# Kernel tuning notes

Hardware: AMD Instinct MI355X
Metric: run time of the kernel (lower is better)

## Reference

```python
import jax, jax.numpy as jnp
import numpy as np

LN_EPS = 1e-5


def _make_valid_boxes(key, shape):
    # boxes in [x_min, y_min, x_max, y_max] with min < max
    k1, k2 = jax.random.split(key)
    mins = jax.random.uniform(k1, shape, dtype=jnp.float32)            # [.., 2]
    sizes = jax.random.uniform(k2, shape, dtype=jnp.float32) * 0.2 + 1e-3
    return jnp.concatenate([mins, mins + sizes], axis=-1)


def setup_inputs() -> dict:
    key = jax.random.key(0)
    k_t, k_b, k_w = jax.random.split(key, 3)
    N, H = 100000, 768
    target = _make_valid_boxes(k_t, (2,))          # [4]
    ocr_boxes = _make_valid_boxes(k_b, (N, 2))     # [N, 4]
    W = jax.random.normal(k_w, (11, H), dtype=jnp.float32) * (1.0 / np.sqrt(11))
    b = jnp.zeros((H,), dtype=jnp.float32)
    ln_gamma = jnp.ones((H,), dtype=jnp.float32)
    ln_beta = jnp.zeros((H,), dtype=jnp.float32)
    return {"target": target, "ocr_boxes": ocr_boxes, "W": W, "b": b,
            "ln_gamma": ln_gamma, "ln_beta": ln_beta}


def _geo_features(target, boxes):
    # target: [4], boxes: [N, 4]  (x_min, y_min, x_max, y_max)
    tx0, ty0, tx1, ty1 = target[0], target[1], target[2], target[3]
    x0, y0, x1, y1 = boxes[:, 0], boxes[:, 1], boxes[:, 2], boxes[:, 3]
    N = boxes.shape[0]
    ones = jnp.ones((N,), boxes.dtype)

    # HeightWidthRelation: [w1, h1, w2, h2, |w1-w2|, |h1-h2|]
    w1, h1 = tx1 - tx0, ty1 - ty0
    w2, h2 = x1 - x0, y1 - y0
    hw = jnp.stack([w1 * ones, h1 * ones, w2, h2,
                    jnp.abs(w1 - w2), jnp.abs(h1 - h2)], axis=-1)   # [N, 6]

    # Centers
    c1x, c1y = (tx0 + tx1) * 0.5, (ty0 + ty1) * 0.5
    c2x, c2y = (x0 + x1) * 0.5, (y0 + y1) * 0.5
    dx, dy = c2x - c1x, c2y - c1y

    # DistanceRelation: L2 center distance
    dist = jnp.sqrt(dx * dx + dy * dy)                               # [N]

    # IoURelation
    overlap = (tx0 < x1) & (tx1 > x0) & (ty0 < y1) & (ty1 > y0)
    xi0, yi0 = jnp.maximum(tx0, x0), jnp.maximum(ty0, y0)
    xi1, yi1 = jnp.minimum(tx1, x1), jnp.minimum(ty1, y1)
    inter = jnp.where(overlap, (xi1 - xi0) * (yi1 - yi0), 0.0)       # [N]
    a1 = w1 * h1
    a2 = w2 * h2
    union = a1 + a2 - inter
    iou = jnp.stack([inter / union, inter / a1, inter / a2], axis=-1)  # [N, 3]

    # AngleRelation: atan2(|dy|, |dx|) degree bucket (degree in [0, 90])
    degree = jnp.arctan2(jnp.abs(dy), jnp.abs(dx)) * (180.0 / jnp.pi)
    bucket = jnp.where((degree > 22.5) & (degree <= 67.5), 1.0,
             jnp.where((degree > 67.5) & (degree <= 112.5), 2.0,
             jnp.where((degree > 112.5) & (degree <= 157.5), 3.0,
             jnp.where((degree > 157.5) & (degree <= 202.5), 4.0,
             jnp.where((degree > 202.5) & (degree <= 247.5), 5.0,
             jnp.where((degree > 247.5) & (degree <= 292.5), 6.0,
             jnp.where((degree > 292.5) & (degree <= 337.5), 7.0, 8.0)))))))

    return jnp.concatenate([hw, dist[:, None], iou, bucket[:, None]], axis=-1)  # [N, 11]


def reference(target, ocr_boxes, W, b, ln_gamma, ln_beta):
    feats = _geo_features(target, ocr_boxes)            # [N, 11]
    x = feats @ W + b                                   # [N, H]
    mean = jnp.mean(x, axis=-1, keepdims=True)
    var = jnp.mean(jnp.square(x - mean), axis=-1, keepdims=True)
    x = (x - mean) * jax.lax.rsqrt(var + LN_EPS) * ln_gamma + ln_beta
    return jax.nn.relu(x)
```

## Files before the change

kernel.cpp:

```cpp
#include <hip/hip_runtime.h>
#include <math.h>

#define H 768
#define LN_EPS 1e-5f

typedef float nfloat4 __attribute__((ext_vector_type(4)));

__device__ __forceinline__ void geo_feats(
    const float4 bx,
    const float tx0, const float ty0, const float tx1, const float ty1,
    const float w1, const float h1, const float c1x, const float c1y,
    const float a1, const float ra1,
    float* __restrict__ v)
{
    const float tanA = 0.41421356237309503f;
    const float tanB = 2.41421356237309503f;
    const float x0 = bx.x, y0 = bx.y, x1 = bx.z, y1 = bx.w;
    const float w2 = x1 - x0, h2 = y1 - y0;
    v[0] = w2; v[1] = h2;
    v[2] = fabsf(w1 - w2); v[3] = fabsf(h1 - h2);
    const float c2x = (x0 + x1) * 0.5f, c2y = (y0 + y1) * 0.5f;
    const float dx = c2x - c1x, dy = c2y - c1y;
    v[4] = __builtin_amdgcn_sqrtf(dx * dx + dy * dy);
    const bool overlap = (tx0 < x1) && (tx1 > x0) && (ty0 < y1) && (ty1 > y0);
    const float xi0 = fmaxf(tx0, x0), yi0 = fmaxf(ty0, y0);
    const float xi1 = fminf(tx1, x1), yi1 = fminf(ty1, y1);
    const float inter = overlap ? (xi1 - xi0) * (yi1 - yi0) : 0.0f;
    const float a2 = w2 * h2;
    const float uni = a1 + a2 - inter;
    v[5] = inter * __builtin_amdgcn_rcpf(uni);
    v[6] = inter * ra1;
    v[7] = inter * __builtin_amdgcn_rcpf(a2);
    const float adx = fabsf(dx), ady = fabsf(dy);
    v[8] = (ady > adx * tanA) ? ((ady > adx * tanB) ? 2.0f : 1.0f) : 8.0f;
}

__global__ __launch_bounds__(256) void gram_kernel(
    const float* __restrict__ W,
    const float* __restrict__ bias,
    float* __restrict__ ws)
{
    const int i = blockIdx.x;
    const int tid = threadIdx.x;

    int p = 0, q = 0;
    const float* A;
    const float* B = nullptr;
    if (i < 78) {
        while ((p + 1) * (p + 2) / 2 <= i) ++p;
        q = i - p * (p + 1) / 2;
        A = (p < 11) ? (W + p * H) : bias;
        B = (q < 11) ? (W + q * H) : bias;
    } else {
        p = i - 78;
        A = (p < 11) ? (W + p * H) : bias;
    }

    float acc = 0.0f;
    if (B) {
        for (int c = tid; c < H; c += 256) acc += A[c] * B[c];
    } else {
        for (int c = tid; c < H; c += 256) acc += A[c];
    }

    #pragma unroll
    for (int off = 32; off >= 1; off >>= 1) acc += __shfl_xor(acc, off, 64);

    __shared__ float red[4];
    if ((tid & 63) == 0) red[tid >> 6] = acc;
    __syncthreads();
    if (tid == 0) {
        const float s = ((red[0] + red[1]) + (red[2] + red[3])) * (1.0f / H);
        if (i < 78) { ws[p * 12 + q] = s; ws[q * 12 + p] = s; }
        else        { ws[144 + p] = s; }
    }
}

__global__ __launch_bounds__(256) void stats_kernel(
    const float* __restrict__ target,
    const float* __restrict__ boxes,
    const float* __restrict__ ws,
    float2* __restrict__ stats,
    int N)
{
    const float tx0 = target[0], ty0 = target[1], tx1 = target[2], ty1 = target[3];
    const float w1 = tx1 - tx0, h1 = ty1 - ty0;
    const float c1x = (tx0 + tx1) * 0.5f, c1y = (ty0 + ty1) * 0.5f;
    const float a1 = w1 * h1;
    const float ra1 = 1.0f / a1;

    float Q[9][9], qlin[9], mlin[9];
    #pragma unroll
    for (int l = 0; l < 9; ++l)
        #pragma unroll
        for (int k = 0; k < 9; ++k)
            Q[l][k] = ws[(l + 2) * 12 + (k + 2)];
    #pragma unroll
    for (int k = 0; k < 9; ++k) {
        qlin[k] = 2.0f * (w1 * ws[0 * 12 + (k + 2)]
                        + h1 * ws[1 * 12 + (k + 2)]
                        +      ws[11 * 12 + (k + 2)]);
        mlin[k] = ws[144 + k + 2];
    }
    const float K = w1 * w1 * ws[0] + 2.0f * w1 * h1 * ws[1] + h1 * h1 * ws[13]
                  + 2.0f * w1 * ws[11] + 2.0f * h1 * ws[1 * 12 + 11] + ws[11 * 12 + 11];
    const float mconst = w1 * ws[144] + h1 * ws[145] + ws[155];

    const float4* __restrict__ boxes4 = reinterpret_cast<const float4*>(boxes);
    const int stride = gridDim.x * blockDim.x;
    for (int b = blockIdx.x * blockDim.x + threadIdx.x; b < N; b += stride) {
        const float4 bx = boxes4[b];
        float v[9];
        geo_feats(bx, tx0, ty0, tx1, ty1, w1, h1, c1x, c1y, a1, ra1, v);

        float mean = mconst;
        #pragma unroll
        for (int k = 0; k < 9; ++k) mean = fmaf(mlin[k], v[k], mean);

        float E = K;
        #pragma unroll
        for (int l = 0; l < 9; ++l) {
            float t = qlin[l];
            #pragma unroll
            for (int k = 0; k < 9; ++k) t = fmaf(Q[l][k], v[k], t);
            E = fmaf(t, v[l], E);
        }

        const float var  = fmaf(-mean, mean, E);
        const float rstd = __builtin_amdgcn_rsqf(fmaxf(var, 0.0f) + LN_EPS);
        float2 st; st.x = rstd; st.y = mean * rstd;
        stats[b] = st;
    }
}

__global__ __launch_bounds__(256, 2) void geo_ln_kernel(
    const float* __restrict__ target,
    const float* __restrict__ boxes,
    const float* __restrict__ W,
    const float* __restrict__ bias,
    const float* __restrict__ gamma,
    const float* __restrict__ beta,
    const float2* __restrict__ stats,
    float* __restrict__ out,
    int N)
{
    const int lane = threadIdx.x & 63;
    const int wid  = (blockIdx.x << 2) | (threadIdx.x >> 6);
    const int nw   = gridDim.x << 2;

    const float tx0 = target[0], ty0 = target[1], tx1 = target[2], ty1 = target[3];
    const float w1 = tx1 - tx0, h1 = ty1 - ty0;
    const float c1x = (tx0 + tx1) * 0.5f, c1y = (ty0 + ty1) * 0.5f;
    const float a1 = w1 * h1;
    const float ra1 = 1.0f / a1;

    const float4* __restrict__ W4  = reinterpret_cast<const float4*>(W);
    const float4* __restrict__ b4  = reinterpret_cast<const float4*>(bias);
    const float4* __restrict__ g4  = reinterpret_cast<const float4*>(gamma);
    const float4* __restrict__ be4 = reinterpret_cast<const float4*>(beta);
    const float4* __restrict__ boxes4 = reinterpret_cast<const float4*>(boxes);
    nfloat4* __restrict__ outv = reinterpret_cast<nfloat4*>(out);

    float4 base[3], Wr[3][9], gm[3], bt[3];
    #pragma unroll
    for (int r = 0; r < 3; ++r) {
        const int c4 = lane + 64 * r;
        float4 acc = b4[c4];
        const float4 w0  = W4[0 * (H / 4) + c4];
        const float4 w1r = W4[1 * (H / 4) + c4];
        acc.x = fmaf(w1, w0.x, acc.x); acc.y = fmaf(w1, w0.y, acc.y);
        acc.z = fmaf(w1, w0.z, acc.z); acc.w = fmaf(w1, w0.w, acc.w);
        acc.x = fmaf(h1, w1r.x, acc.x); acc.y = fmaf(h1, w1r.y, acc.y);
        acc.z = fmaf(h1, w1r.z, acc.z); acc.w = fmaf(h1, w1r.w, acc.w);
        base[r] = acc;
        #pragma unroll
        for (int k = 0; k < 9; ++k)
            Wr[r][k] = W4[(k + 2) * (H / 4) + c4];
        gm[r] = g4[c4];
        bt[r] = be4[c4];
    }

    auto process = [&](const float4 bx, const float2 st, const int box) {
        float v[9];
        geo_feats(bx, tx0, ty0, tx1, ty1, w1, h1, c1x, c1y, a1, ra1, v);
        const float rstd = st.x;
        const float nmr  = -st.y;
        nfloat4* __restrict__ orow = outv + (size_t)box * (H / 4);
        #pragma unroll
        for (int r = 0; r < 3; ++r) {
            float4 acc = base[r];
            #pragma unroll
            for (int k = 0; k < 9; ++k) {
                const float4 w = Wr[r][k];
                acc.x = fmaf(v[k], w.x, acc.x);
                acc.y = fmaf(v[k], w.y, acc.y);
                acc.z = fmaf(v[k], w.z, acc.z);
                acc.w = fmaf(v[k], w.w, acc.w);
            }
            const float4 g = gm[r], be = bt[r];
            nfloat4 o;
            o.x = fmaxf(0.0f, fmaf(fmaf(acc.x, rstd, nmr), g.x, be.x));
            o.y = fmaxf(0.0f, fmaf(fmaf(acc.y, rstd, nmr), g.y, be.y));
            o.z = fmaxf(0.0f, fmaf(fmaf(acc.z, rstd, nmr), g.z, be.z));
            o.w = fmaxf(0.0f, fmaf(fmaf(acc.w, rstd, nmr), g.w, be.w));
            __builtin_nontemporal_store(o, &orow[lane + 64 * r]);
        }
    };

    int box = wid;
    if (box >= N) return;
    float4 bA = boxes4[box];
    float2 sA = stats[box];
    bool hasB = (box + nw < N);
    float4 bB = bA; float2 sB = sA;
    if (hasB) { bB = boxes4[box + nw]; sB = stats[box + nw]; }

    while (hasB) {
        const int nxt = box + 2 * nw;
        const bool hA = (nxt < N), hB = (nxt + nw < N);
        float4 nA = bA, nB = bB; float2 nsA = sA, nsB = sB;
        if (hA) { nA = boxes4[nxt];      nsA = stats[nxt]; }
        if (hB) { nB = boxes4[nxt + nw]; nsB = stats[nxt + nw]; }
        process(bA, sA, box);
        process(bB, sB, box + nw);
        bA = nA; sA = nsA; bB = nB; sB = nsB;
        box = nxt; hasB = hB;
    }
    if (box < N) process(bA, sA, box);
}

__global__ __launch_bounds__(256, 2) void geo_ln_fallback(
    const float* __restrict__ target,
    const float* __restrict__ boxes,
    const float* __restrict__ W,
    const float* __restrict__ bias,
    const float* __restrict__ gamma,
    const float* __restrict__ beta,
    float* __restrict__ out,
    int N)
{
    const int lane = threadIdx.x & 63;
    const int wid  = (blockIdx.x << 2) | (threadIdx.x >> 6);
    const int nw   = gridDim.x << 2;

    const float tx0 = target[0], ty0 = target[1], tx1 = target[2], ty1 = target[3];
    const float w1 = tx1 - tx0, h1 = ty1 - ty0;
    const float c1x = (tx0 + tx1) * 0.5f, c1y = (ty0 + ty1) * 0.5f;
    const float a1 = w1 * h1;
    const float ra1 = 1.0f / a1;

    const float4* __restrict__ W4  = reinterpret_cast<const float4*>(W);
    const float4* __restrict__ b4  = reinterpret_cast<const float4*>(bias);
    const float4* __restrict__ g4  = reinterpret_cast<const float4*>(gamma);
    const float4* __restrict__ be4 = reinterpret_cast<const float4*>(beta);
    const float4* __restrict__ boxes4 = reinterpret_cast<const float4*>(boxes);
    nfloat4* __restrict__ outv = reinterpret_cast<nfloat4*>(out);

    float4 base[3], Wr[3][9], gm[3], bt[3];
    #pragma unroll
    for (int r = 0; r < 3; ++r) {
        const int c4 = lane + 64 * r;
        float4 acc = b4[c4];
        const float4 w0  = W4[0 * (H / 4) + c4];
        const float4 w1r = W4[1 * (H / 4) + c4];
        acc.x = fmaf(w1, w0.x, acc.x); acc.y = fmaf(w1, w0.y, acc.y);
        acc.z = fmaf(w1, w0.z, acc.z); acc.w = fmaf(w1, w0.w, acc.w);
        acc.x = fmaf(h1, w1r.x, acc.x); acc.y = fmaf(h1, w1r.y, acc.y);
        acc.z = fmaf(h1, w1r.z, acc.z); acc.w = fmaf(h1, w1r.w, acc.w);
        base[r] = acc;
        #pragma unroll
        for (int k = 0; k < 9; ++k)
            Wr[r][k] = W4[(k + 2) * (H / 4) + c4];
        gm[r] = g4[c4];
        bt[r] = be4[c4];
    }

    auto process = [&](int box) {
        const float4 bx = boxes4[box];
        float v[9];
        geo_feats(bx, tx0, ty0, tx1, ty1, w1, h1, c1x, c1y, a1, ra1, v);

        float4 xv[3];
        float s = 0.0f, sq = 0.0f;
        #pragma unroll
        for (int r = 0; r < 3; ++r) {
            float4 acc = base[r];
            #pragma unroll
            for (int k = 0; k < 9; ++k) {
                const float4 w = Wr[r][k];
                acc.x = fmaf(v[k], w.x, acc.x);
                acc.y = fmaf(v[k], w.y, acc.y);
                acc.z = fmaf(v[k], w.z, acc.z);
                acc.w = fmaf(v[k], w.w, acc.w);
            }
            xv[r] = acc;
            s  += acc.x + acc.y + acc.z + acc.w;
            sq += acc.x * acc.x + acc.y * acc.y + acc.z * acc.z + acc.w * acc.w;
        }

        #pragma unroll
        for (int off = 32; off >= 1; off >>= 1) {
            s  += __shfl_xor(s,  off, 64);
            sq += __shfl_xor(sq, off, 64);
        }
        const float mean = s * (1.0f / H);
        const float var  = sq * (1.0f / H) - mean * mean;
        const float rstd = __builtin_amdgcn_rsqf(var + LN_EPS);

        nfloat4* __restrict__ orow = outv + (size_t)box * (H / 4);
        #pragma unroll
        for (int r = 0; r < 3; ++r) {
            const float4 vx = xv[r];
            const float4 g = gm[r], be = bt[r];
            nfloat4 o;
            o.x = fmaxf(0.0f, (vx.x - mean) * rstd * g.x + be.x);
            o.y = fmaxf(0.0f, (vx.y - mean) * rstd * g.y + be.y);
            o.z = fmaxf(0.0f, (vx.z - mean) * rstd * g.z + be.z);
            o.w = fmaxf(0.0f, (vx.w - mean) * rstd * g.w + be.w);
            __builtin_nontemporal_store(o, &orow[lane + 64 * r]);
        }
    };

    int box = wid;
    for (; box + nw < N; box += 2 * nw) {
        process(box);
        process(box + nw);
    }
    if (box < N) process(box);
}

extern "C" void kernel_launch(void* const* d_in, const int* in_sizes, int n_in,
                              void* d_out, int out_size, void* d_ws, size_t ws_size,
                              hipStream_t stream) {
    const float* target = (const float*)d_in[0];
    const float* boxes  = (const float*)d_in[1];
    const float* W      = (const float*)d_in[2];
    const float* bias   = (const float*)d_in[3];
    const float* gamma  = (const float*)d_in[4];
    const float* beta   = (const float*)d_in[5];
    float* out = (float*)d_out;

    const int N = in_sizes[1] / 4;

    const size_t needed = (160 + 2 * (size_t)N) * sizeof(float);

    if (d_ws && ws_size >= needed && N > 0) {
        float* wsf = (float*)d_ws;
        float2* stats = (float2*)(wsf + 160);

        gram_kernel<<<90, 256, 0, stream>>>(W, bias, wsf);

        int blocksA2 = (N + 255) / 256;
        if (blocksA2 > 2048) blocksA2 = 2048;
        stats_kernel<<<blocksA2, 256, 0, stream>>>(target, boxes, wsf, stats, N);

        geo_ln_kernel<<<512, 256, 0, stream>>>(target, boxes, W, bias, gamma, beta,
                                               stats, out, N);
    } else {
        geo_ln_fallback<<<512, 256, 0, stream>>>(target, boxes, W, bias, gamma, beta,
                                                 out, N);
    }
}
```

Measured before the change: 324.5 us.

## Split each row across three waves by column slice with LDS-staged box records

The main kernel now assigns each wavefront one third of the 768 output columns (role) for a fixed strided set of boxes, instead of one wave computing all columns of a row. This cuts per-thread weight registers to a third, which allows higher occupancy (launch bounds 4, 1536 blocks). Each wave preloads its box coordinates and LN stats into shared memory before the main loop, so the loop no longer issues global loads. Each wave recomputes the geometric features for its boxes, tripling that work, and the path is limited to N <= 2048*64; larger N falls back to the slower kernel.

```diff
diff --git a/kernel.cpp b/kernel.cpp
--- a/kernel.cpp
+++ b/kernel.cpp
@@ -3,6 +3,7 @@
 
 #define H 768
 #define LN_EPS 1e-5f
+#define NTRIP 2048
 
 typedef float nfloat4 __attribute__((ext_vector_type(4)));
 
@@ -133,7 +134,7 @@
     }
 }
 
-__global__ __launch_bounds__(256, 2) void geo_ln_kernel(
+__global__ __launch_bounds__(256, 4) void geo_ln_main(
     const float* __restrict__ target,
     const float* __restrict__ boxes,
     const float* __restrict__ W,
@@ -145,8 +146,10 @@
     int N)
 {
     const int lane = threadIdx.x & 63;
-    const int wid  = (blockIdx.x << 2) | (threadIdx.x >> 6);
-    const int nw   = gridDim.x << 2;
+    const int wl   = threadIdx.x >> 6;
+    const int g    = (blockIdx.x << 2) | wl;
+    const int t    = g / 3;
+    const int role = g - 3 * t;
 
     const float tx0 = target[0], ty0 = target[1], tx1 = target[2], ty1 = target[3];
     const float w1 = tx1 - tx0, h1 = ty1 - ty0;
@@ -161,72 +164,64 @@
     const float4* __restrict__ boxes4 = reinterpret_cast<const float4*>(boxes);
     nfloat4* __restrict__ outv = reinterpret_cast<nfloat4*>(out);
 
-    float4 base[3], Wr[3][9], gm[3], bt[3];
-    #pragma unroll
-    for (int r = 0; r < 3; ++r) {
-        const int c4 = lane + 64 * r;
-        float4 acc = b4[c4];
+    const int c4 = lane + (role << 6);
+    float4 base = b4[c4];
+    {
         const float4 w0  = W4[0 * (H / 4) + c4];
         const float4 w1r = W4[1 * (H / 4) + c4];
-        acc.x = fmaf(w1, w0.x, acc.x); acc.y = fmaf(w1, w0.y, acc.y);
-        acc.z = fmaf(w1, w0.z, acc.z); acc.w = fmaf(w1, w0.w, acc.w);
-        acc.x = fmaf(h1, w1r.x, acc.x); acc.y = fmaf(h1, w1r.y, acc.y);
-        acc.z = fmaf(h1, w1r.z, acc.z); acc.w = fmaf(h1, w1r.w, acc.w);
-        base[r] = acc;
-        #pragma unroll
-        for (int k = 0; k < 9; ++k)
-            Wr[r][k] = W4[(k + 2) * (H / 4) + c4];
-        gm[r] = g4[c4];
-        bt[r] = be4[c4];
-    }
-
-    auto process = [&](const float4 bx, const float2 st, const int box) {
+        base.x = fmaf(w1, w0.x, base.x); base.y = fmaf(w1, w0.y, base.y);
+        base.z = fmaf(w1, w0.z, base.z); base.w = fmaf(w1, w0.w, base.w);
+        base.x = fmaf(h1, w1r.x, base.x); base.y = fmaf(h1, w1r.y, base.y);
+        base.z = fmaf(h1, w1r.z, base.z); base.w = fmaf(h1, w1r.w, base.w);
+    }
+    float4 Wr[9];
+    #pragma unroll
+    for (int k = 0; k < 9; ++k) Wr[k] = W4[(k + 2) * (H / 4) + c4];
+    const float4 gm = g4[c4];
+    const float4 bt = be4[c4];
+
+    __shared__ float recs[4][64 * 8];
+    const int nb = (t < N) ? ((N - t + NTRIP - 1) / NTRIP) : 0;
+    for (int l = lane; l < nb; l += 64) {
+        const int b = t + l * NTRIP;
+        const float4 bx = boxes4[b];
+        const float2 st = stats[b];
+        float* r = &recs[wl][l * 8];
+        r[0] = bx.x; r[1] = bx.y; r[2] = bx.z; r[3] = bx.w;
+        r[4] = st.x; r[5] = st.y;
+    }
+    __syncthreads();
+
+    const float* rw = recs[wl];
+    nfloat4* op = outv + (size_t)t * (H / 4) + c4;
+    const size_t ostep = (size_t)NTRIP * (H / 4);
+
+    #pragma unroll 2
+    for (int k = 0; k < nb; ++k) {
+        const float4 bx = *reinterpret_cast<const float4*>(rw + k * 8);
+        const float rstd = rw[k * 8 + 4];
+        const float nmr  = -rw[k * 8 + 5];
+
         float v[9];
         geo_feats(bx, tx0, ty0, tx1, ty1, w1, h1, c1x, c1y, a1, ra1, v);
-        const float rstd = st.x;
-        const float nmr  = -st.y;
-        nfloat4* __restrict__ orow = outv + (size_t)box * (H / 4);
-        #pragma unroll
-        for (int r = 0; r < 3; ++r) {
-            float4 acc = base[r];
-            #pragma unroll
-            for (int k = 0; k < 9; ++k) {
-                const float4 w = Wr[r][k];
-                acc.x = fmaf(v[k], w.x, acc.x);
-                acc.y = fmaf(v[k], w.y, acc.y);
-                acc.z = fmaf(v[k], w.z, acc.z);
-                acc.w = fmaf(v[k], w.w, acc.w);
-            }
-            const float4 g = gm[r], be = bt[r];
-            nfloat4 o;
-            o.x = fmaxf(0.0f, fmaf(fmaf(acc.x, rstd, nmr), g.x, be.x));
-            o.y = fmaxf(0.0f, fmaf(fmaf(acc.y, rstd, nmr), g.y, be.y));
-            o.z = fmaxf(0.0f, fmaf(fmaf(acc.z, rstd, nmr), g.z, be.z));
-            o.w = fmaxf(0.0f, fmaf(fmaf(acc.w, rstd, nmr), g.w, be.w));
-            __builtin_nontemporal_store(o, &orow[lane + 64 * r]);
-        }
-    };
-
-    int box = wid;
-    if (box >= N) return;
-    float4 bA = boxes4[box];
-    float2 sA = stats[box];
-    bool hasB = (box + nw < N);
-    float4 bB = bA; float2 sB = sA;
-    if (hasB) { bB = boxes4[box + nw]; sB = stats[box + nw]; }
-
-    while (hasB) {
-        const int nxt = box + 2 * nw;
-        const bool hA = (nxt < N), hB = (nxt + nw < N);
-        float4 nA = bA, nB = bB; float2 nsA = sA, nsB = sB;
-        if (hA) { nA = boxes4[nxt];      nsA = stats[nxt]; }
-        if (hB) { nB = boxes4[nxt + nw]; nsB = stats[nxt + nw]; }
-        process(bA, sA, box);
-        process(bB, sB, box + nw);
-        bA = nA; sA = nsA; bB = nB; sB = nsB;
-        box = nxt; hasB = hB;
-    }
-    if (box < N) process(bA, sA, box);
+
+        float4 acc = base;
+        #pragma unroll
+        for (int j = 0; j < 9; ++j) {
+            const float4 w = Wr[j];
+            acc.x = fmaf(v[j], w.x, acc.x);
+            acc.y = fmaf(v[j], w.y, acc.y);
+            acc.z = fmaf(v[j], w.z, acc.z);
+            acc.w = fmaf(v[j], w.w, acc.w);
+        }
+        nfloat4 o;
+        o.x = fmaxf(0.0f, fmaf(fmaf(acc.x, rstd, nmr), gm.x, bt.x));
+        o.y = fmaxf(0.0f, fmaf(fmaf(acc.y, rstd, nmr), gm.y, bt.y));
+        o.z = fmaxf(0.0f, fmaf(fmaf(acc.z, rstd, nmr), gm.z, bt.z));
+        o.w = fmaxf(0.0f, fmaf(fmaf(acc.w, rstd, nmr), gm.w, bt.w));
+        __builtin_nontemporal_store(o, op);
+        op += ostep;
+    }
 }
 
 __global__ __launch_bounds__(256, 2) void geo_ln_fallback(
@@ -343,8 +338,9 @@
     const int N = in_sizes[1] / 4;
 
     const size_t needed = (160 + 2 * (size_t)N) * sizeof(float);
-
-    if (d_ws && ws_size >= needed && N > 0) {
+    const bool stats_ok = d_ws && ws_size >= needed && N > 0 && N <= NTRIP * 64;
+
+    if (stats_ok) {
         float* wsf = (float*)d_ws;
         float2* stats = (float2*)(wsf + 160);
 
@@ -354,8 +350,8 @@
         if (blocksA2 > 2048) blocksA2 = 2048;
         stats_kernel<<<blocksA2, 256, 0, stream>>>(target, boxes, wsf, stats, N);
 
-        geo_ln_kernel<<<512, 256, 0, stream>>>(target, boxes, W, bias, gamma, beta,
-                                               stats, out, N);
+        geo_ln_main<<<1536, 256, 0, stream>>>(target, boxes, W, bias, gamma, beta,
+                                              stats, out, N);
     } else {
         geo_ln_fallback<<<512, 256, 0, stream>>>(target, boxes, W, bias, gamma, beta,
                                                  out, N);
```

New measurement: 321.8 us. No clear change (-0.8%).
